# Optimization experiments

Hardware: AMD Instinct MI355X
Metric: run time of the kernel (lower is better)

The kernel has to match this reference:

```python
import jax, jax.numpy as jnp
import numpy as np

HEADS = 5 - 1  # 4 attention heads (GPSConv heads=4)


def _bn(x, g, b, eps=1e-5):
    # BatchNorm1d, training-mode math (biased variance), matches torch normalization
    mu = x.mean(0)
    var = x.var(0)
    return g * (x - mu) * jax.lax.rsqrt(var + eps) + b


def _forward(x, t, freqs, t_fc1_W, t_fc1_b, t_fc2_W, t_fc2_b, node_W, node_b,
             tproj_W, tproj_b, tcat_W, tcat_b, pen_g, pen_b, pel_W, pel_b,
             cat_W, cat_b, conv_Wg, gru_Wih, gru_bih, gru_Whh, gru_bhh,
             attn_Wqkv, attn_bqkv, attn_Wo, attn_bo, bn_g, bn_b,
             mlp_W1, mlp_b1, mlp_W2, mlp_b2, out_W, out_b):
    B, C, Hh, Ww = x.shape
    HD = node_W.shape[1]          # hidden_dim = 64
    DH = HD // HEADS              # per-head dim = 16
    WL = pen_g.shape[0]           # walk_length = 20

    xf = x.reshape(B, -1)                              # [B, D]
    h = xf @ node_W + node_b                           # node_proj

    # TimeEmbedding: t @ freqs -> sin/cos -> MLP, then time_proj
    tp = t.reshape(B, 1) * freqs.reshape(1, -1)        # [B, nf]
    two_pi = jnp.asarray(2.0 * np.pi, x.dtype)
    te = jnp.concatenate([jnp.sin(two_pi * tp), jnp.cos(two_pi * tp)], axis=-1)
    te = jax.nn.silu(te @ t_fc1_W + t_fc1_b) @ t_fc2_W + t_fc2_b
    h_time = te @ tproj_W + tproj_b
    h = jnp.concatenate([h, h_time], axis=-1) @ tcat_W + tcat_b  # time_cat_proj

    # Fully-connected graph incl. self-loops: A = 1 everywhere, deg = B.
    # Random-walk PE: P = A/deg has all entries 1/B; P is idempotent (P@P = P),
    # hence diag(P^k) = diag(P) = 1/B for every k in 1..walk_length.
    A = jnp.ones((B, B), x.dtype)
    P = A / A.sum(1, keepdims=True)
    pe = jnp.broadcast_to(jnp.diagonal(P)[:, None], (B, WL))
    pe = _bn(pe, pen_g, pen_b)                         # pe_norm (batch stats)
    h = jnp.concatenate([h, pe @ pel_W + pel_b], axis=-1) @ cat_W + cat_b

    inv_sqrt = jnp.asarray(1.0 / np.sqrt(DH), x.dtype)
    for l in range(conv_Wg.shape[0]):                  # 5 GPSConv layers
        # --- GatedGraphConv (num_layers=1): message, add-aggregate, GRU ---
        m = A @ (h @ conv_Wg[l])                       # sum of messages from all src nodes
        gi = m @ gru_Wih[l] + gru_bih[l]               # [B, 3H]
        gh = h @ gru_Whh[l] + gru_bhh[l]
        ir, iz, inn = jnp.split(gi, 3, axis=-1)
        hr, hz, hn = jnp.split(gh, 3, axis=-1)
        r = jax.nn.sigmoid(ir + hr)
        z = jax.nn.sigmoid(iz + hz)
        n = jnp.tanh(inn + r * hn)
        hc = (1.0 - z) * n + z * h                     # GRUCell output
        h1 = _bn(hc + h, bn_g[l, 0], bn_b[l, 0])       # residual + norm1

        # --- global multihead self-attention over the single dense batch ---
        qkv = h @ attn_Wqkv[l] + attn_bqkv[l]
        q, k, v = jnp.split(qkv, 3, axis=-1)
        q = q.reshape(B, HEADS, DH).transpose(1, 0, 2)  # [h, B, d]
        k = k.reshape(B, HEADS, DH).transpose(1, 0, 2)
        v = v.reshape(B, HEADS, DH).transpose(1, 0, 2)
        att = jax.nn.softmax(jnp.einsum('hqd,hkd->hqk', q, k) * inv_sqrt, axis=-1)
        o = jnp.einsum('hqk,hkd->hqd', att, v).transpose(1, 0, 2).reshape(B, HD)
        o = o @ attn_Wo[l] + attn_bo[l]
        h2 = _bn(o + h, bn_g[l, 1], bn_b[l, 1])        # residual + norm2

        s = h1 + h2
        s = s + (jax.nn.relu(s @ mlp_W1[l] + mlp_b1[l]) @ mlp_W2[l] + mlp_b2[l])
        h = _bn(s, bn_g[l, 2], bn_b[l, 2])             # norm3

    return (h @ out_W + out_b).reshape(B, C, Hh, Ww)


def setup_inputs() -> dict:
    key = jax.random.key(0)
    B, C, H, W = 2048, 4, 32, 32
    D = C * H * W                 # 4096
    HD, PE, WL, L = 64, 16, 20, 5
    NF, TH, TC = 8, 64, 64
    ks = iter(jax.random.split(key, 40))

    def rn(shape, s=0.05):
        return jax.random.normal(next(ks), shape, jnp.float32) * s

    return {
        'x': jax.random.normal(next(ks), (B, C, H, W), jnp.float32),
        't': jax.random.uniform(next(ks), (B,), jnp.float32),
        'freqs': rn((NF,), 1.0),
        't_fc1_W': rn((2 * NF, TH)), 't_fc1_b': rn((TH,)),
        't_fc2_W': rn((TH, TC)), 't_fc2_b': rn((TC,)),
        'node_W': rn((D, HD), 0.02), 'node_b': rn((HD,)),
        'tproj_W': rn((TC, HD)), 'tproj_b': rn((HD,)),
        'tcat_W': rn((2 * HD, HD)), 'tcat_b': rn((HD,)),
        'pen_g': jnp.ones((WL,), jnp.float32), 'pen_b': jnp.zeros((WL,), jnp.float32),
        'pel_W': rn((WL, PE)), 'pel_b': rn((PE,)),
        'cat_W': rn((HD + PE, HD)), 'cat_b': rn((HD,)),
        'conv_Wg': rn((L, HD, HD)),
        'gru_Wih': rn((L, HD, 3 * HD)), 'gru_bih': rn((L, 3 * HD)),
        'gru_Whh': rn((L, HD, 3 * HD)), 'gru_bhh': rn((L, 3 * HD)),
        'attn_Wqkv': rn((L, HD, 3 * HD)), 'attn_bqkv': rn((L, 3 * HD)),
        'attn_Wo': rn((L, HD, HD)), 'attn_bo': rn((L, HD)),
        'bn_g': jnp.ones((L, 3, HD), jnp.float32), 'bn_b': jnp.zeros((L, 3, HD), jnp.float32),
        'mlp_W1': rn((L, HD, 2 * HD)), 'mlp_b1': rn((L, 2 * HD)),
        'mlp_W2': rn((L, 2 * HD, HD)), 'mlp_b2': rn((L, HD)),
        'out_W': rn((HD, D)), 'out_b': rn((D,)),
    }


def reference(x, t, freqs, t_fc1_W, t_fc1_b, t_fc2_W, t_fc2_b, node_W, node_b,
              tproj_W, tproj_b, tcat_W, tcat_b, pen_g, pen_b, pel_W, pel_b,
              cat_W, cat_b, conv_Wg, gru_Wih, gru_bih, gru_Whh, gru_bhh,
              attn_Wqkv, attn_bqkv, attn_Wo, attn_bo, bn_g, bn_b,
              mlp_W1, mlp_b1, mlp_W2, mlp_b2, out_W, out_b):
    return _forward(x, t, freqs, t_fc1_W, t_fc1_b, t_fc2_W, t_fc2_b, node_W, node_b,
                    tproj_W, tproj_b, tcat_W, tcat_b, pen_g, pen_b, pel_W, pel_b,
                    cat_W, cat_b, conv_Wg, gru_Wih, gru_bih, gru_Whh, gru_bhh,
                    attn_Wqkv, attn_bqkv, attn_Wo, attn_bo, bn_g, bn_b,
                    mlp_W1, mlp_b1, mlp_W2, mlp_b2, out_W, out_b)
```

## Files before the change

### kernel.cpp

```cpp
#include <hip/hip_runtime.h>

#define NB 2048
#define HDM 64
#define NLAY 5

typedef __bf16 bf16x8 __attribute__((ext_vector_type(8)));
typedef float v4f __attribute__((ext_vector_type(4)));

__device__ __forceinline__ float sigmoidf_(float x){ return 1.f/(1.f+__expf(-x)); }
__device__ __forceinline__ float tanhfast_(float x){
  x = fminf(fmaxf(x, -15.f), 15.f);
  float e = __expf(2.f*x);
  return (e-1.f)/(e+1.f);
}
__device__ __forceinline__ unsigned short f2b_rne(float f){
  unsigned u = __float_as_uint(f);
  unsigned r = u + 0x7FFFu + ((u>>16)&1u);
  return (unsigned short)(r>>16);
}
__device__ __forceinline__ unsigned pk2(float a, float b){
  unsigned ua = (__float_as_uint(a) + 0x8000u) >> 16;
  unsigned ub = (__float_as_uint(b) + 0x8000u) & 0xFFFF0000u;
  return ua | ub;
}

__global__ __launch_bounds__(256) void k_pre(
    const float* __restrict__ x, const float* __restrict__ tt,
    const float* __restrict__ freqs,
    const float* __restrict__ fc1W, const float* __restrict__ fc1b,
    const float* __restrict__ fc2W, const float* __restrict__ fc2b,
    const float* __restrict__ tprojW, const float* __restrict__ tprojb,
    const float* __restrict__ nodeW,
    float* __restrict__ h0p, float* __restrict__ htime,
    float* __restrict__ zero_region)
{
  __shared__ float xsT[256*20];
  __shared__ float tb0[128];
  __shared__ float tb1[128];
  const int t = threadIdx.x, blk = blockIdx.x;
  const int r = t>>6, c = t&63;

  if (blk == 0){
    for (int i = t; i < 320 + 1920; i += 256) zero_region[i] = 0.f;
  }

  {
    const int row = blk*2 + (r&1);
    const float tv = tt[row];
    if (r < 2){
      float te[16];
      #pragma unroll
      for (int j=0;j<8;++j){
        float sv, cv;
        __sincosf(6.28318530717958647692f*tv*freqs[j], &sv, &cv);
        te[j]=sv; te[j+8]=cv;
      }
      float a = fc1b[c];
      #pragma unroll
      for (int j=0;j<16;++j) a += te[j]*fc1W[j*64+c];
      tb0[r*64+c] = a*sigmoidf_(a);
    }
    __syncthreads();
    if (r < 2){
      float b2 = fc2b[c];
      #pragma unroll 8
      for (int k=0;k<64;++k) b2 += tb0[r*64+k]*fc2W[k*64+c];
      tb1[r*64+c] = b2;
    }
    __syncthreads();
    if (r < 2){
      float hti = tprojb[c];
      #pragma unroll 8
      for (int k=0;k<64;++k) hti += tb1[r*64+k]*tprojW[k*64+c];
      htime[row*64+c] = hti;
    }
  }

  const int rg = blk>>3, kq = blk&7;
  const int rows0 = rg*16, k0 = kq*512;
  const int col4 = (t&15)*4;
  const int rq4  = ((t>>4)&3)*4;
  const int ksub = (t>>6)*64;

  float4 a0={0,0,0,0}, a1={0,0,0,0}, a2={0,0,0,0}, a3={0,0,0,0};

  for (int ch=0; ch<2; ++ch){
    __syncthreads();
    #pragma unroll
    for (int i=0;i<4;++i){
      int fi = t + 256*i;
      int xr = fi>>6, kk = (fi&63)<<2;
      float4 xv = *(const float4*)&x[(size_t)(rows0+xr)*4096 + k0 + ch*256 + kk];
      xsT[(kk+0)*20+xr]=xv.x; xsT[(kk+1)*20+xr]=xv.y;
      xsT[(kk+2)*20+xr]=xv.z; xsT[(kk+3)*20+xr]=xv.w;
    }
    __syncthreads();
    const float* wp = &nodeW[(size_t)(k0 + ch*256 + ksub)*64 + col4];
    const float* xp = &xsT[ksub*20 + rq4];
    #pragma unroll 8
    for (int kk=0; kk<64; ++kk){
      float4 w  = *(const float4*)&wp[kk*64];
      float4 xr4 = *(const float4*)&xp[kk*20];
      a0.x += xr4.x*w.x; a0.y += xr4.x*w.y; a0.z += xr4.x*w.z; a0.w += xr4.x*w.w;
      a1.x += xr4.y*w.x; a1.y += xr4.y*w.y; a1.z += xr4.y*w.z; a1.w += xr4.y*w.w;
      a2.x += xr4.z*w.x; a2.y += xr4.z*w.y; a2.z += xr4.z*w.z; a2.w += xr4.z*w.w;
      a3.x += xr4.w*w.x; a3.y += xr4.w*w.y; a3.z += xr4.w*w.z; a3.w += xr4.w*w.w;
    }
  }
  __syncthreads();
  {
    const int kqi = t>>6;
    *(float4*)&xsT[(kqi*16 + rq4 + 0)*64 + col4] = a0;
    *(float4*)&xsT[(kqi*16 + rq4 + 1)*64 + col4] = a1;
    *(float4*)&xsT[(kqi*16 + rq4 + 2)*64 + col4] = a2;
    *(float4*)&xsT[(kqi*16 + rq4 + 3)*64 + col4] = a3;
  }
  __syncthreads();
  {
    const int row = t>>4, c4 = (t&15)*4;
    float4 s = {0,0,0,0};
    #pragma unroll
    for (int q=0;q<4;++q){
      float4 v = *(const float4*)&xsT[(q*16+row)*64 + c4];
      s.x+=v.x; s.y+=v.y; s.z+=v.z; s.w+=v.w;
    }
    *(float4*)&h0p[(size_t)kq*(NB*HDM) + (rows0+row)*64 + c4] = s;
  }
}

__global__ __launch_bounds__(256) void k_assemble(
    const float* __restrict__ h0p, const float* __restrict__ htime,
    const float* __restrict__ nodeb,
    const float* __restrict__ tcatW, const float* __restrict__ tcatb,
    const float* __restrict__ penb, const float* __restrict__ pelW,
    const float* __restrict__ pelb,
    const float* __restrict__ catW, const float* __restrict__ catb,
    float* __restrict__ hbuf)
{
  __shared__ float sa[256];
  __shared__ float sb[256];
  __shared__ float cvec[64];
  const int t = threadIdx.x, blk = blockIdx.x;
  const int r = t>>6, c = t&63;
  const int row = blk*4 + r;

  if (r==0){
    float pl[16];
    #pragma unroll
    for (int j=0;j<16;++j){
      float a = pelb[j];
      for (int w=0;w<20;++w) a += penb[w]*pelW[w*16+j];
      pl[j]=a;
    }
    float a = catb[c];
    #pragma unroll
    for (int j=0;j<16;++j) a += pl[j]*catW[(64+j)*64+c];
    cvec[c]=a;
  }
  float h0 = nodeb[c];
  #pragma unroll
  for (int q=0;q<8;++q) h0 += h0p[(size_t)q*(NB*HDM) + row*64 + c];
  sa[t] = h0;
  sb[t] = htime[row*64+c];
  __syncthreads();
  float a = tcatb[c];
  #pragma unroll 4
  for (int k=0;k<64;++k){
    a += sa[r*64+k]*tcatW[k*64+c];
    a += sb[r*64+k]*tcatW[(64+k)*64+c];
  }
  __syncthreads();
  sa[t] = a;
  __syncthreads();
  float hv = cvec[c];
  #pragma unroll 8
  for (int k=0;k<64;++k) hv += sa[r*64+k]*catW[k*64+c];
  hbuf[row*64+c] = hv;
}

__global__ __launch_bounds__(256) void k_A(
    const float* __restrict__ smlp,
    const float* __restrict__ bnaccPrev,
    const float* __restrict__ gPrev, const float* __restrict__ bPrev,
    float* __restrict__ hbuf, float* __restrict__ hsumL,
    const float* __restrict__ Whh, const float* __restrict__ bhh,
    const float* __restrict__ Wq,  const float* __restrict__ bq,
    float* __restrict__ gh,
    unsigned short* __restrict__ Qb, unsigned short* __restrict__ Kb,
    unsigned short* __restrict__ Vt, int first)
{
  __shared__ float sa[256];
  const int t = threadIdx.x, blk = blockIdx.x;
  const int r = t>>6, c = t&63;
  const int row0 = blk*4;
  const int row = row0 + r;

  float hv;
  if (first){
    hv = hbuf[row*64+c];
  } else {
    float mu = bnaccPrev[256+c]*(1.f/NB);
    float va = bnaccPrev[320+c]*(1.f/NB) - mu*mu;
    hv = gPrev[c]*(smlp[row*64+c]-mu)*rsqrtf(va+1e-5f)+bPrev[c];
    hbuf[row*64+c] = hv;
  }
  sa[t] = hv;
  __syncthreads();
  if (t<64){
    atomicAdd(&hsumL[t], sa[t]+sa[64+t]+sa[128+t]+sa[192+t]);
  }
  int rrA[3], ccA[3];
  float ag[3], aq[3];
  #pragma unroll
  for (int i=0;i<3;++i){
    int idx = t + 256*i;
    rrA[i] = idx/192; ccA[i] = idx - rrA[i]*192;
    ag[i] = bhh[ccA[i]]; aq[i] = bq[ccA[i]];
  }
  #pragma unroll 4
  for (int k=0;k<64;++k){
    #pragma unroll
    for (int i=0;i<3;++i){
      float hk = sa[rrA[i]*64+k];
      ag[i] += hk*Whh[k*192+ccA[i]];
      aq[i] += hk*Wq [k*192+ccA[i]];
    }
  }
  #pragma unroll
  for (int i=0;i<3;++i){
    int rw = row0 + rrA[i], cc = ccA[i];
    gh[(size_t)rw*192+cc] = ag[i];
    float aqv = aq[i];
    if (cc < 64){
      int hd = cc>>4, dh = cc&15;
      size_t base = ((size_t)(hd<<11) + rw)*32;
      Qb[base+dh] = f2b_rne(aqv*0.25f);
      Qb[base+16+dh] = 0;
    } else if (cc < 128){
      int c2 = cc-64, hd = c2>>4, dh = c2&15;
      size_t base = ((size_t)(hd<<11) + rw)*32;
      Kb[base+dh] = f2b_rne(aqv);
      Kb[base+16+dh] = 0;
    } else {
      int c2 = cc-128, hd = c2>>4, dh = c2&15;
      Vt[((size_t)(hd*16+dh))*2048 + rw] = f2b_rne(aqv);
    }
  }
}

__global__ __launch_bounds__(64) void k_attn(
    const unsigned short* __restrict__ Qb, const unsigned short* __restrict__ Kb,
    const unsigned short* __restrict__ Vt,
    float* __restrict__ Upart, float* __restrict__ mpart, float* __restrict__ lpart)
{
  __shared__ unsigned short Pl[16*40];
  const int lane = threadIdx.x;
  const int q15 = lane & 15, quad = lane >> 4;
  const int b = blockIdx.x;
  const int qt = b & 127, head = (b>>7)&3, part = b>>9;
  const int qrow = qt*16 + q15;
  const int key00 = part*512;

  const bf16x8 qf = *(const bf16x8*)&Qb[(((size_t)(head<<11))+qrow)*32 + quad*8];
  const unsigned short* Kb_h = Kb + ((size_t)(head<<11))*32;
  const unsigned short* Vrow = Vt + ((size_t)(head*16+q15))*2048;

  v4f O = {0.f,0.f,0.f,0.f};
  float m = -1e30f, lsum = 0.f;

  bf16x8 kf0 = *(const bf16x8*)&Kb_h[(size_t)(key00 + q15)*32 + quad*8];
  bf16x8 kf1 = *(const bf16x8*)&Kb_h[(size_t)(key00 + 16 + q15)*32 + quad*8];
  bf16x8 vf  = *(const bf16x8*)&Vrow[key00 + quad*8];

  for (int c=0; c<16; ++c){
    bf16x8 nk0, nk1, nv;
    if (c < 15){
      int nk = key00 + (c+1)*32;
      nk0 = *(const bf16x8*)&Kb_h[(size_t)(nk + q15)*32 + quad*8];
      nk1 = *(const bf16x8*)&Kb_h[(size_t)(nk + 16 + q15)*32 + quad*8];
      nv  = *(const bf16x8*)&Vrow[nk + quad*8];
    }
    v4f z = {0.f,0.f,0.f,0.f};
    v4f s0 = __builtin_amdgcn_mfma_f32_16x16x32_bf16(kf0, qf, z, 0,0,0);
    v4f s1 = __builtin_amdgcn_mfma_f32_16x16x32_bf16(kf1, qf, z, 0,0,0);
    float cmax = fmaxf(fmaxf(fmaxf(s0[0],s0[1]),fmaxf(s0[2],s0[3])),
                       fmaxf(fmaxf(s1[0],s1[1]),fmaxf(s1[2],s1[3])));
    cmax = fmaxf(cmax, __shfl_xor(cmax,16,64));
    cmax = fmaxf(cmax, __shfl_xor(cmax,32,64));
    float mnew = fmaxf(m, cmax);
    float alpha = __expf(m - mnew);
    float p0=__expf(s0[0]-mnew), p1=__expf(s0[1]-mnew), p2=__expf(s0[2]-mnew), p3=__expf(s0[3]-mnew);
    float p4=__expf(s1[0]-mnew), p5=__expf(s1[1]-mnew), p6=__expf(s1[2]-mnew), p7=__expf(s1[3]-mnew);
    lsum = alpha*lsum + ((p0+p1)+(p2+p3)+((p4+p5)+(p6+p7)));
    m = mnew;
    O[0]*=alpha; O[1]*=alpha; O[2]*=alpha; O[3]*=alpha;
    *(uint2*)&Pl[q15*40 + quad*4]      = make_uint2(pk2(p0,p1), pk2(p2,p3));
    *(uint2*)&Pl[q15*40 + 16 + quad*4] = make_uint2(pk2(p4,p5), pk2(p6,p7));
    __syncthreads();
    bf16x8 pf = *(const bf16x8*)&Pl[q15*40 + quad*8];
    O = __builtin_amdgcn_mfma_f32_16x16x32_bf16(vf, pf, O, 0,0,0);
    kf0 = nk0; kf1 = nk1; vf = nv;
  }
  lsum += __shfl_xor(lsum,16,64);
  lsum += __shfl_xor(lsum,32,64);
  size_t ub = ((size_t)((part*4+head)*2048) + qrow)*16 + quad*4;
  *(float4*)&Upart[ub] = make_float4(O[0],O[1],O[2],O[3]);
  if (quad==0){
    mpart[(size_t)(part*4+head)*2048 + qrow] = m;
    lpart[(size_t)(part*4+head)*2048 + qrow] = lsum;
  }
}

__global__ __launch_bounds__(256) void k_B2(
    const float* __restrict__ hbuf, const float* __restrict__ gh,
    const float* __restrict__ hsumL,
    const float* __restrict__ Upart, const float* __restrict__ mpart,
    const float* __restrict__ lpart,
    const float* __restrict__ Wg,   const float* __restrict__ Wih,
    const float* __restrict__ bih,  const float* __restrict__ Wo,
    const float* __restrict__ bo,
    float* __restrict__ s1, float* __restrict__ s2, float* __restrict__ bnaccL)
{
  __shared__ float sa[256];
  __shared__ float os[256];
  __shared__ float smv_[64];
  __shared__ float sgi[192];
  __shared__ float Sb[512];
  const int t = threadIdx.x, blk = blockIdx.x;
  const int r = t>>6, c = t&63;
  const int row = blk*4 + r;
  const int head = c>>4, dh = c&15;

  if (t<64){
    float a=0.f;
    #pragma unroll 8
    for (int k=0;k<64;++k) a += hsumL[k]*Wg[k*64+t];
    smv_[t]=a;
  }
  sa[t] = hbuf[row*64+c];

  float m0 = mpart[(size_t)(head)*2048+row],    m1 = mpart[(size_t)(4+head)*2048+row];
  float m2 = mpart[(size_t)(8+head)*2048+row],  m3 = mpart[(size_t)(12+head)*2048+row];
  float mm = fmaxf(fmaxf(m0,m1),fmaxf(m2,m3));
  float a0=__expf(m0-mm), a1=__expf(m1-mm), a2=__expf(m2-mm), a3=__expf(m3-mm);
  float ll = a0*lpart[(size_t)(head)*2048+row]   + a1*lpart[(size_t)(4+head)*2048+row]
           + a2*lpart[(size_t)(8+head)*2048+row] + a3*lpart[(size_t)(12+head)*2048+row];
  float uu = a0*Upart[((size_t)(head)*2048+row)*16+dh]    + a1*Upart[((size_t)(4+head)*2048+row)*16+dh]
           + a2*Upart[((size_t)(8+head)*2048+row)*16+dh]  + a3*Upart[((size_t)(12+head)*2048+row)*16+dh];
  os[t] = uu / ll;
  __syncthreads();
  if (t<192){
    float a = bih[t];
    #pragma unroll 8
    for (int k=0;k<64;++k) a += smv_[k]*Wih[k*192+t];
    sgi[t]=a;
  }
  __syncthreads();

  float o2 = bo[c];
  #pragma unroll 8
  for (int k=0;k<64;++k) o2 += os[r*64+k]*Wo[k*64+c];
  float hv = sa[t];
  float s2v = o2 + hv;
  float ir = sgi[c]      + gh[(size_t)row*192+c];
  float iz = sgi[64+c]   + gh[(size_t)row*192+64+c];
  float inn = sgi[128+c];
  float hn  = gh[(size_t)row*192+128+c];
  float rr_ = sigmoidf_(ir);
  float zz  = sigmoidf_(iz);
  float nn  = tanhfast_(inn + rr_*hn);
  float s1v = (1.f-zz)*nn + zz*hv + hv;
  s1[row*64+c] = s1v;
  s2[row*64+c] = s2v;
  Sb[t] = s1v; Sb[256+t] = s2v;
  __syncthreads();
  if (t<64){
    float a=0.f,aq=0.f,b=0.f,bq2=0.f;
    #pragma unroll
    for (int rr=0;rr<4;++rr){
      float v1 = Sb[rr*64+t], v2 = Sb[256+rr*64+t];
      a+=v1; aq+=v1*v1; b+=v2; bq2+=v2*v2;
    }
    atomicAdd(&bnaccL[t],a);     atomicAdd(&bnaccL[64+t],aq);
    atomicAdd(&bnaccL[128+t],b); atomicAdd(&bnaccL[192+t],bq2);
  }
}

__global__ __launch_bounds__(256) void k_C(
    const float* __restrict__ s1, const float* __restrict__ s2,
    const float* __restrict__ bngL, const float* __restrict__ bnbL,
    const float* __restrict__ W1, const float* __restrict__ b1,
    const float* __restrict__ W2, const float* __restrict__ b2,
    float* __restrict__ smlp, float* __restrict__ bnaccL)
{
  __shared__ float sa[256];
  __shared__ float sh[512];
  __shared__ float S2[256];
  const int t = threadIdx.x, blk = blockIdx.x;
  const int r = t>>6, c = t&63;
  const int row = blk*4 + r;

  float mu1 = bnaccL[c]*(1.f/NB);
  float va1 = bnaccL[64+c]*(1.f/NB) - mu1*mu1;
  float mu2 = bnaccL[128+c]*(1.f/NB);
  float va2 = bnaccL[192+c]*(1.f/NB) - mu2*mu2;
  float h1 = bngL[c]*(s1[row*64+c]-mu1)*rsqrtf(va1+1e-5f)+bnbL[c];
  float h2 = bngL[64+c]*(s2[row*64+c]-mu2)*rsqrtf(va2+1e-5f)+bnbL[64+c];
  float sv = h1+h2;
  sa[t]=sv;
  __syncthreads();
  {
    const int rr0 = t>>7, hj0 = t&127;
    const int idx1 = t + 256;
    const int rr1 = idx1>>7, hj1 = idx1&127;
    float a0v = b1[hj0], a1v = b1[hj1];
    #pragma unroll 4
    for (int k=0;k<64;++k){
      a0v += sa[rr0*64+k]*W1[k*128+hj0];
      a1v += sa[rr1*64+k]*W1[k*128+hj1];
    }
    sh[t] = fmaxf(a0v, 0.f);
    sh[t+256] = fmaxf(a1v, 0.f);
  }
  __syncthreads();
  float mo = b2[c];
  #pragma unroll 8
  for (int k=0;k<128;++k) mo += sh[r*128+k]*W2[k*64+c];
  float smv2 = sv + mo;
  smlp[row*64+c]=smv2;
  S2[t]=smv2;
  __syncthreads();
  if (t<64){
    float a=0.f,aq=0.f;
    #pragma unroll
    for (int rr=0;rr<4;++rr){ float v=S2[rr*64+t]; a+=v; aq+=v*v; }
    atomicAdd(&bnaccL[256+t],a); atomicAdd(&bnaccL[320+t],aq);
  }
}

__global__ __launch_bounds__(256) void k_out(
  const float* __restrict__ smlp, const float* __restrict__ bnacc4,
  const float* __restrict__ g4, const float* __restrict__ b4,
  const float* __restrict__ outW, const float* __restrict__ outb,
  float* __restrict__ out)
{
  __shared__ float hsT[64*20];
  const int t = threadIdx.x, blk = blockIdx.x;
  const int rg = blk>>2, cg = blk&3;
  const int rows0 = rg*16;
  #pragma unroll
  for (int i=0;i<4;++i){
    int idx = t + 256*i;
    int k = idx&63, rr = idx>>6;
    float mu = bnacc4[256+k]*(1.f/NB);
    float va = bnacc4[320+k]*(1.f/NB)-mu*mu;
    hsT[k*20+rr] = g4[k]*(smlp[(size_t)(rows0+rr)*64+k]-mu)*rsqrtf(va+1e-5f)+b4[k];
  }
  __syncthreads();
  for (int j=0;j<4;++j){
    int cc = cg*1024 + t + 256*j;
    float acc[16];
    float bv = outb[cc];
    #pragma unroll
    for (int rr=0;rr<16;++rr) acc[rr]=bv;
    #pragma unroll 4
    for (int k=0;k<64;++k){
      float w = outW[(size_t)k*4096+cc];
      const float4* hp = (const float4*)&hsT[k*20];
      float4 h0=hp[0], h1=hp[1], h2=hp[2], h3=hp[3];
      acc[0]+=h0.x*w;  acc[1]+=h0.y*w;  acc[2]+=h0.z*w;  acc[3]+=h0.w*w;
      acc[4]+=h1.x*w;  acc[5]+=h1.y*w;  acc[6]+=h1.z*w;  acc[7]+=h1.w*w;
      acc[8]+=h2.x*w;  acc[9]+=h2.y*w;  acc[10]+=h2.z*w; acc[11]+=h2.w*w;
      acc[12]+=h3.x*w; acc[13]+=h3.y*w; acc[14]+=h3.z*w; acc[15]+=h3.w*w;
    }
    #pragma unroll
    for (int rr=0;rr<16;++rr) out[(size_t)(rows0+rr)*4096+cc]=acc[rr];
  }
}

extern "C" void kernel_launch(void* const* d_in, const int* in_sizes, int n_in,
                              void* d_out, int out_size, void* d_ws, size_t ws_size,
                              hipStream_t stream)
{
  (void)in_sizes; (void)n_in; (void)out_size; (void)ws_size;
  const float* x      = (const float*)d_in[0];
  const float* tt     = (const float*)d_in[1];
  const float* freqs  = (const float*)d_in[2];
  const float* fc1W   = (const float*)d_in[3];
  const float* fc1b   = (const float*)d_in[4];
  const float* fc2W   = (const float*)d_in[5];
  const float* fc2b   = (const float*)d_in[6];
  const float* nodeW  = (const float*)d_in[7];
  const float* nodeb  = (const float*)d_in[8];
  const float* tprojW = (const float*)d_in[9];
  const float* tprojb = (const float*)d_in[10];
  const float* tcatW  = (const float*)d_in[11];
  const float* tcatb  = (const float*)d_in[12];
  const float* penb   = (const float*)d_in[14];
  const float* pelW   = (const float*)d_in[15];
  const float* pelb   = (const float*)d_in[16];
  const float* catW   = (const float*)d_in[17];
  const float* catb   = (const float*)d_in[18];
  const float* convWg = (const float*)d_in[19];
  const float* gruWih = (const float*)d_in[20];
  const float* grubih = (const float*)d_in[21];
  const float* gruWhh = (const float*)d_in[22];
  const float* grubhh = (const float*)d_in[23];
  const float* Wqkv   = (const float*)d_in[24];
  const float* bqkv   = (const float*)d_in[25];
  const float* Wo     = (const float*)d_in[26];
  const float* bo     = (const float*)d_in[27];
  const float* bng    = (const float*)d_in[28];
  const float* bnb    = (const float*)d_in[29];
  const float* W1     = (const float*)d_in[30];
  const float* b1     = (const float*)d_in[31];
  const float* W2     = (const float*)d_in[32];
  const float* b2     = (const float*)d_in[33];
  const float* outW   = (const float*)d_in[34];
  const float* outb   = (const float*)d_in[35];

  float* ws = (float*)d_ws;
  float* htime = ws;
  float* hbuf  = htime + 131072;
  float* gh    = hbuf + 131072;
  float* s1    = gh + 393216;
  float* s2    = s1 + 131072;
  float* smlp  = s2 + 131072;
  float* hsum  = smlp + 131072;
  float* bnacc = hsum + 320;
  float* Upart = bnacc + 1920;
  float* mpart = Upart + 524288;
  float* lpart = mpart + 32768;
  unsigned short* Qb = (unsigned short*)(lpart + 32768);
  unsigned short* Kb = Qb + 262144;
  unsigned short* Vt = Kb + 262144;
  float* h0p = Upart;

  dim3 G(512), Blk(256);

  k_pre<<<dim3(1024), Blk, 0, stream>>>(x, tt, freqs, fc1W, fc1b, fc2W, fc2b,
                                        tprojW, tprojb, nodeW, h0p, htime, hsum);

  k_assemble<<<G, Blk, 0, stream>>>(h0p, htime, nodeb, tcatW, tcatb,
                                    penb, pelW, pelb, catW, catb, hbuf);

  for (int l=0; l<NLAY; ++l){
    const float* bnaccPrev = (l==0) ? bnacc : bnacc + (l-1)*384;
    const float* gPrev = (l==0) ? bng : bng + (l-1)*192 + 128;
    const float* bPrev = (l==0) ? bnb : bnb + (l-1)*192 + 128;
    k_A<<<G, Blk, 0, stream>>>(smlp, bnaccPrev, gPrev, bPrev,
                               hbuf, hsum + l*64,
                               gruWhh + l*12288, grubhh + l*192,
                               Wqkv + l*12288, bqkv + l*192,
                               gh, Qb, Kb, Vt, (l==0) ? 1 : 0);
    k_attn<<<dim3(2048), dim3(64), 0, stream>>>(Qb, Kb, Vt, Upart, mpart, lpart);
    k_B2<<<G, Blk, 0, stream>>>(hbuf, gh, hsum + l*64, Upart, mpart, lpart,
                                convWg + l*4096, gruWih + l*12288, grubih + l*192,
                                Wo + l*4096, bo + l*64,
                                s1, s2, bnacc + l*384);
    k_C<<<G, Blk, 0, stream>>>(s1, s2, bng + l*192, bnb + l*192,
                               W1 + l*8192, b1 + l*128, W2 + l*8192, b2 + l*64,
                               smlp, bnacc + l*384);
  }

  k_out<<<G, Blk, 0, stream>>>(smlp, bnacc + 4*384, bng + 896, bnb + 896,
                               outW, outb, (float*)d_out);
}
```

Baseline: 612.1 us.

## Merge attention split-K in-block, widen row tiles, vectorize node and output GEMMs

Attention now runs the four key partitions as four waves of one 256-thread block and combines the partial softmax results in shared memory, writing normalized outputs directly. This removes the Upart/mpart/lpart round trip through global memory and the combine step in k_B2. k_A, k_B2 and k_C now handle 8 rows per block so each weight load is reused across more rows, at the cost of half as many blocks. k_pre stores x row-major in shared memory instead of transposing it, and k_out uses float4 weight loads and stores. Register pressure rises in the reworked loops, and the lower block counts may leave some compute units idle.

New measurement: 523.5 us. -14.5%, faster.

```diff
diff --git a/kernel.cpp b/kernel.cpp
--- a/kernel.cpp
+++ b/kernel.cpp
@@ -34,7 +34,7 @@
     float* __restrict__ h0p, float* __restrict__ htime,
     float* __restrict__ zero_region)
 {
-  __shared__ float xsT[256*20];
+  __shared__ float xs[16*260];
   __shared__ float tb0[128];
   __shared__ float tb1[128];
   const int t = threadIdx.x, blk = blockIdx.x;
@@ -90,30 +90,31 @@
     for (int i=0;i<4;++i){
       int fi = t + 256*i;
       int xr = fi>>6, kk = (fi&63)<<2;
-      float4 xv = *(const float4*)&x[(size_t)(rows0+xr)*4096 + k0 + ch*256 + kk];
-      xsT[(kk+0)*20+xr]=xv.x; xsT[(kk+1)*20+xr]=xv.y;
-      xsT[(kk+2)*20+xr]=xv.z; xsT[(kk+3)*20+xr]=xv.w;
+      *(float4*)&xs[xr*260+kk] = *(const float4*)&x[(size_t)(rows0+xr)*4096 + k0 + ch*256 + kk];
     }
     __syncthreads();
     const float* wp = &nodeW[(size_t)(k0 + ch*256 + ksub)*64 + col4];
-    const float* xp = &xsT[ksub*20 + rq4];
+    const float* xp = &xs[rq4*260 + ksub];
     #pragma unroll 8
     for (int kk=0; kk<64; ++kk){
       float4 w  = *(const float4*)&wp[kk*64];
-      float4 xr4 = *(const float4*)&xp[kk*20];
-      a0.x += xr4.x*w.x; a0.y += xr4.x*w.y; a0.z += xr4.x*w.z; a0.w += xr4.x*w.w;
-      a1.x += xr4.y*w.x; a1.y += xr4.y*w.y; a1.z += xr4.y*w.z; a1.w += xr4.y*w.w;
-      a2.x += xr4.z*w.x; a2.y += xr4.z*w.y; a2.z += xr4.z*w.z; a2.w += xr4.z*w.w;
-      a3.x += xr4.w*w.x; a3.y += xr4.w*w.y; a3.z += xr4.w*w.z; a3.w += xr4.w*w.w;
+      float x0 = xp[kk];
+      float x1 = xp[260+kk];
+      float x2 = xp[520+kk];
+      float x3 = xp[780+kk];
+      a0.x += x0*w.x; a0.y += x0*w.y; a0.z += x0*w.z; a0.w += x0*w.w;
+      a1.x += x1*w.x; a1.y += x1*w.y; a1.z += x1*w.z; a1.w += x1*w.w;
+      a2.x += x2*w.x; a2.y += x2*w.y; a2.z += x2*w.z; a2.w += x2*w.w;
+      a3.x += x3*w.x; a3.y += x3*w.y; a3.z += x3*w.z; a3.w += x3*w.w;
     }
   }
   __syncthreads();
   {
     const int kqi = t>>6;
-    *(float4*)&xsT[(kqi*16 + rq4 + 0)*64 + col4] = a0;
-    *(float4*)&xsT[(kqi*16 + rq4 + 1)*64 + col4] = a1;
-    *(float4*)&xsT[(kqi*16 + rq4 + 2)*64 + col4] = a2;
-    *(float4*)&xsT[(kqi*16 + rq4 + 3)*64 + col4] = a3;
+    *(float4*)&xs[(kqi*16 + rq4 + 0)*64 + col4] = a0;
+    *(float4*)&xs[(kqi*16 + rq4 + 1)*64 + col4] = a1;
+    *(float4*)&xs[(kqi*16 + rq4 + 2)*64 + col4] = a2;
+    *(float4*)&xs[(kqi*16 + rq4 + 3)*64 + col4] = a3;
   }
   __syncthreads();
   {
@@ -121,7 +122,7 @@
     float4 s = {0,0,0,0};
     #pragma unroll
     for (int q=0;q<4;++q){
-      float4 v = *(const float4*)&xsT[(q*16+row)*64 + c4];
+      float4 v = *(const float4*)&xs[(q*16+row)*64 + c4];
       s.x+=v.x; s.y+=v.y; s.z+=v.z; s.w+=v.w;
     }
     *(float4*)&h0p[(size_t)kq*(NB*HDM) + (rows0+row)*64 + c4] = s;
@@ -189,77 +190,89 @@
     unsigned short* __restrict__ Qb, unsigned short* __restrict__ Kb,
     unsigned short* __restrict__ Vt, int first)
 {
-  __shared__ float sa[256];
+  __shared__ float sa[8*64];
   const int t = threadIdx.x, blk = blockIdx.x;
-  const int r = t>>6, c = t&63;
-  const int row0 = blk*4;
-  const int row = row0 + r;
-
-  float hv;
-  if (first){
-    hv = hbuf[row*64+c];
-  } else {
-    float mu = bnaccPrev[256+c]*(1.f/NB);
-    float va = bnaccPrev[320+c]*(1.f/NB) - mu*mu;
-    hv = gPrev[c]*(smlp[row*64+c]-mu)*rsqrtf(va+1e-5f)+bPrev[c];
-    hbuf[row*64+c] = hv;
-  }
-  sa[t] = hv;
+  const int row0 = blk*8;
+
+  #pragma unroll
+  for (int i=0;i<2;++i){
+    int idx = t + 256*i;
+    int rl = idx>>6, c = idx&63;
+    int row = row0 + rl;
+    float hv;
+    if (first){
+      hv = hbuf[row*64+c];
+    } else {
+      float mu = bnaccPrev[256+c]*(1.f/NB);
+      float va = bnaccPrev[320+c]*(1.f/NB) - mu*mu;
+      hv = gPrev[c]*(smlp[row*64+c]-mu)*rsqrtf(va+1e-5f)+bPrev[c];
+      hbuf[row*64+c] = hv;
+    }
+    sa[idx] = hv;
+  }
   __syncthreads();
   if (t<64){
-    atomicAdd(&hsumL[t], sa[t]+sa[64+t]+sa[128+t]+sa[192+t]);
-  }
-  int rrA[3], ccA[3];
-  float ag[3], aq[3];
-  #pragma unroll
-  for (int i=0;i<3;++i){
-    int idx = t + 256*i;
-    rrA[i] = idx/192; ccA[i] = idx - rrA[i]*192;
-    ag[i] = bhh[ccA[i]]; aq[i] = bq[ccA[i]];
-  }
-  #pragma unroll 4
-  for (int k=0;k<64;++k){
-    #pragma unroll
-    for (int i=0;i<3;++i){
-      float hk = sa[rrA[i]*64+k];
-      ag[i] += hk*Whh[k*192+ccA[i]];
-      aq[i] += hk*Wq [k*192+ccA[i]];
-    }
-  }
-  #pragma unroll
-  for (int i=0;i<3;++i){
-    int rw = row0 + rrA[i], cc = ccA[i];
-    gh[(size_t)rw*192+cc] = ag[i];
-    float aqv = aq[i];
-    if (cc < 64){
-      int hd = cc>>4, dh = cc&15;
-      size_t base = ((size_t)(hd<<11) + rw)*32;
-      Qb[base+dh] = f2b_rne(aqv*0.25f);
-      Qb[base+16+dh] = 0;
-    } else if (cc < 128){
-      int c2 = cc-64, hd = c2>>4, dh = c2&15;
-      size_t base = ((size_t)(hd<<11) + rw)*32;
-      Kb[base+dh] = f2b_rne(aqv);
-      Kb[base+16+dh] = 0;
-    } else {
-      int c2 = cc-128, hd = c2>>4, dh = c2&15;
-      Vt[((size_t)(hd*16+dh))*2048 + rw] = f2b_rne(aqv);
-    }
-  }
-}
-
-__global__ __launch_bounds__(64) void k_attn(
+    float s = 0.f;
+    #pragma unroll
+    for (int rl=0;rl<8;++rl) s += sa[rl*64+t];
+    atomicAdd(&hsumL[t], s);
+  }
+  if (t < 192){
+    const int cc = t;
+    float ag[8], aq[8];
+    float bh = bhh[cc], bq_ = bq[cc];
+    #pragma unroll
+    for (int rl=0;rl<8;++rl){ ag[rl]=bh; aq[rl]=bq_; }
+    #pragma unroll 4
+    for (int k=0;k<64;++k){
+      float wh = Whh[k*192+cc];
+      float wq = Wq [k*192+cc];
+      #pragma unroll
+      for (int rl=0;rl<8;++rl){
+        float hk = sa[rl*64+k];
+        ag[rl] += hk*wh;
+        aq[rl] += hk*wq;
+      }
+    }
+    #pragma unroll
+    for (int rl=0;rl<8;++rl){
+      int rw = row0 + rl;
+      gh[(size_t)rw*192+cc] = ag[rl];
+      float aqv = aq[rl];
+      if (cc < 64){
+        int hd = cc>>4, dh = cc&15;
+        size_t base = ((size_t)(hd<<11) + rw)*32;
+        Qb[base+dh] = f2b_rne(aqv*0.25f);
+        Qb[base+16+dh] = 0;
+      } else if (cc < 128){
+        int c2 = cc-64, hd = c2>>4, dh = c2&15;
+        size_t base = ((size_t)(hd<<11) + rw)*32;
+        Kb[base+dh] = f2b_rne(aqv);
+        Kb[base+16+dh] = 0;
+      } else {
+        int c2 = cc-128, hd = c2>>4, dh = c2&15;
+        Vt[((size_t)(hd*16+dh))*2048 + rw] = f2b_rne(aqv);
+      }
+    }
+  }
+}
+
+__global__ __launch_bounds__(256) void k_attn(
     const unsigned short* __restrict__ Qb, const unsigned short* __restrict__ Kb,
     const unsigned short* __restrict__ Vt,
-    float* __restrict__ Upart, float* __restrict__ mpart, float* __restrict__ lpart)
-{
-  __shared__ unsigned short Pl[16*40];
-  const int lane = threadIdx.x;
+    float* __restrict__ o_out)
+{
+  __shared__ unsigned short Pl[4*640];
+  __shared__ float Os[4*272];
+  __shared__ float ms[64], ls[64];
+  const int t = threadIdx.x;
+  const int w = t>>6, lane = t&63;
   const int q15 = lane & 15, quad = lane >> 4;
   const int b = blockIdx.x;
-  const int qt = b & 127, head = (b>>7)&3, part = b>>9;
+  const int qt = b & 127, head = b>>7;
   const int qrow = qt*16 + q15;
-  const int key00 = part*512;
+  const int key00 = w*512;
+  unsigned short* Plw = &Pl[w*640];
 
   const bf16x8 qf = *(const bf16x8*)&Qb[(((size_t)(head<<11))+qrow)*32 + quad*8];
   const unsigned short* Kb_h = Kb + ((size_t)(head<<11))*32;
@@ -294,42 +307,46 @@
     lsum = alpha*lsum + ((p0+p1)+(p2+p3)+((p4+p5)+(p6+p7)));
     m = mnew;
     O[0]*=alpha; O[1]*=alpha; O[2]*=alpha; O[3]*=alpha;
-    *(uint2*)&Pl[q15*40 + quad*4]      = make_uint2(pk2(p0,p1), pk2(p2,p3));
-    *(uint2*)&Pl[q15*40 + 16 + quad*4] = make_uint2(pk2(p4,p5), pk2(p6,p7));
-    __syncthreads();
-    bf16x8 pf = *(const bf16x8*)&Pl[q15*40 + quad*8];
+    *(uint2*)&Plw[q15*40 + quad*4]      = make_uint2(pk2(p0,p1), pk2(p2,p3));
+    *(uint2*)&Plw[q15*40 + 16 + quad*4] = make_uint2(pk2(p4,p5), pk2(p6,p7));
+    asm volatile("s_waitcnt lgkmcnt(0)" ::: "memory");
+    bf16x8 pf = *(const bf16x8*)&Plw[q15*40 + quad*8];
     O = __builtin_amdgcn_mfma_f32_16x16x32_bf16(vf, pf, O, 0,0,0);
     kf0 = nk0; kf1 = nk1; vf = nv;
   }
   lsum += __shfl_xor(lsum,16,64);
   lsum += __shfl_xor(lsum,32,64);
-  size_t ub = ((size_t)((part*4+head)*2048) + qrow)*16 + quad*4;
-  *(float4*)&Upart[ub] = make_float4(O[0],O[1],O[2],O[3]);
-  if (quad==0){
-    mpart[(size_t)(part*4+head)*2048 + qrow] = m;
-    lpart[(size_t)(part*4+head)*2048 + qrow] = lsum;
+  #pragma unroll
+  for (int j=0;j<4;++j) Os[w*272 + q15*17 + quad*4 + j] = O[j];
+  if (quad==0){ ms[w*16+q15]=m; ls[w*16+q15]=lsum; }
+  __syncthreads();
+  {
+    const int dh = t&15, q = t>>4;
+    float m0=ms[q], m1=ms[16+q], m2=ms[32+q], m3=ms[48+q];
+    float mm = fmaxf(fmaxf(m0,m1),fmaxf(m2,m3));
+    float a0=__expf(m0-mm), a1=__expf(m1-mm), a2=__expf(m2-mm), a3=__expf(m3-mm);
+    float ll = a0*ls[q]+a1*ls[16+q]+a2*ls[32+q]+a3*ls[48+q];
+    float oo = a0*Os[q*17+dh] + a1*Os[272+q*17+dh] + a2*Os[544+q*17+dh] + a3*Os[816+q*17+dh];
+    o_out[(size_t)(qt*16+q)*64 + head*16 + dh] = oo / ll;
   }
 }
 
 __global__ __launch_bounds__(256) void k_B2(
     const float* __restrict__ hbuf, const float* __restrict__ gh,
-    const float* __restrict__ hsumL,
-    const float* __restrict__ Upart, const float* __restrict__ mpart,
-    const float* __restrict__ lpart,
+    const float* __restrict__ hsumL, const float* __restrict__ o_out,
     const float* __restrict__ Wg,   const float* __restrict__ Wih,
     const float* __restrict__ bih,  const float* __restrict__ Wo,
     const float* __restrict__ bo,
     float* __restrict__ s1, float* __restrict__ s2, float* __restrict__ bnaccL)
 {
-  __shared__ float sa[256];
-  __shared__ float os[256];
+  __shared__ float sa[8*64];
+  __shared__ float os[8*64];
   __shared__ float smv_[64];
   __shared__ float sgi[192];
-  __shared__ float Sb[512];
+  __shared__ float Sb1[8*64];
+  __shared__ float Sb2[8*64];
   const int t = threadIdx.x, blk = blockIdx.x;
-  const int r = t>>6, c = t&63;
-  const int row = blk*4 + r;
-  const int head = c>>4, dh = c&15;
+  const int row0 = blk*8;
 
   if (t<64){
     float a=0.f;
@@ -337,17 +354,13 @@
     for (int k=0;k<64;++k) a += hsumL[k]*Wg[k*64+t];
     smv_[t]=a;
   }
-  sa[t] = hbuf[row*64+c];
-
-  float m0 = mpart[(size_t)(head)*2048+row],    m1 = mpart[(size_t)(4+head)*2048+row];
-  float m2 = mpart[(size_t)(8+head)*2048+row],  m3 = mpart[(size_t)(12+head)*2048+row];
-  float mm = fmaxf(fmaxf(m0,m1),fmaxf(m2,m3));
-  float a0=__expf(m0-mm), a1=__expf(m1-mm), a2=__expf(m2-mm), a3=__expf(m3-mm);
-  float ll = a0*lpart[(size_t)(head)*2048+row]   + a1*lpart[(size_t)(4+head)*2048+row]
-           + a2*lpart[(size_t)(8+head)*2048+row] + a3*lpart[(size_t)(12+head)*2048+row];
-  float uu = a0*Upart[((size_t)(head)*2048+row)*16+dh]    + a1*Upart[((size_t)(4+head)*2048+row)*16+dh]
-           + a2*Upart[((size_t)(8+head)*2048+row)*16+dh]  + a3*Upart[((size_t)(12+head)*2048+row)*16+dh];
-  os[t] = uu / ll;
+  #pragma unroll
+  for (int i=0;i<2;++i){
+    int idx = t + 256*i;
+    int rl = idx>>6, c = idx&63;
+    sa[idx] = hbuf[(size_t)(row0+rl)*64+c];
+    os[idx] = o_out[(size_t)(row0+rl)*64+c];
+  }
   __syncthreads();
   if (t<192){
     float a = bih[t];
@@ -357,28 +370,40 @@
   }
   __syncthreads();
 
-  float o2 = bo[c];
-  #pragma unroll 8
-  for (int k=0;k<64;++k) o2 += os[r*64+k]*Wo[k*64+c];
-  float hv = sa[t];
-  float s2v = o2 + hv;
-  float ir = sgi[c]      + gh[(size_t)row*192+c];
-  float iz = sgi[64+c]   + gh[(size_t)row*192+64+c];
-  float inn = sgi[128+c];
-  float hn  = gh[(size_t)row*192+128+c];
-  float rr_ = sigmoidf_(ir);
-  float zz  = sigmoidf_(iz);
-  float nn  = tanhfast_(inn + rr_*hn);
-  float s1v = (1.f-zz)*nn + zz*hv + hv;
-  s1[row*64+c] = s1v;
-  s2[row*64+c] = s2v;
-  Sb[t] = s1v; Sb[256+t] = s2v;
+  const int c = t&63, rg = t>>6;
+  float o2a = bo[c], o2b = bo[c];
+  #pragma unroll 4
+  for (int k=0;k<64;++k){
+    float w = Wo[k*64+c];
+    o2a += os[(rg*2  )*64+k]*w;
+    o2b += os[(rg*2+1)*64+k]*w;
+  }
+  #pragma unroll
+  for (int i=0;i<2;++i){
+    int rl = rg*2 + i;
+    int row = row0 + rl;
+    float o2 = i ? o2b : o2a;
+    float hv = sa[rl*64+c];
+    float s2v = o2 + hv;
+    float ir = sgi[c]      + gh[(size_t)row*192+c];
+    float iz = sgi[64+c]   + gh[(size_t)row*192+64+c];
+    float inn = sgi[128+c];
+    float hn  = gh[(size_t)row*192+128+c];
+    float rr_ = sigmoidf_(ir);
+    float zz  = sigmoidf_(iz);
+    float nn  = tanhfast_(inn + rr_*hn);
+    float s1v = (1.f-zz)*nn + zz*hv + hv;
+    s1[(size_t)row*64+c] = s1v;
+    s2[(size_t)row*64+c] = s2v;
+    Sb1[rl*64+c] = s1v;
+    Sb2[rl*64+c] = s2v;
+  }
   __syncthreads();
   if (t<64){
     float a=0.f,aq=0.f,b=0.f,bq2=0.f;
     #pragma unroll
-    for (int rr=0;rr<4;++rr){
-      float v1 = Sb[rr*64+t], v2 = Sb[256+rr*64+t];
+    for (int rl=0;rl<8;++rl){
+      float v1 = Sb1[rl*64+t], v2 = Sb2[rl*64+t];
       a+=v1; aq+=v1*v1; b+=v2; bq2+=v2*v2;
     }
     atomicAdd(&bnaccL[t],a);     atomicAdd(&bnaccL[64+t],aq);
@@ -393,47 +418,65 @@
     const float* __restrict__ W2, const float* __restrict__ b2,
     float* __restrict__ smlp, float* __restrict__ bnaccL)
 {
-  __shared__ float sa[256];
-  __shared__ float sh[512];
-  __shared__ float S2[256];
+  __shared__ float sa[8*64];
+  __shared__ float sh[8*128];
+  __shared__ float S2[8*64];
   const int t = threadIdx.x, blk = blockIdx.x;
-  const int r = t>>6, c = t&63;
-  const int row = blk*4 + r;
-
-  float mu1 = bnaccL[c]*(1.f/NB);
-  float va1 = bnaccL[64+c]*(1.f/NB) - mu1*mu1;
-  float mu2 = bnaccL[128+c]*(1.f/NB);
-  float va2 = bnaccL[192+c]*(1.f/NB) - mu2*mu2;
-  float h1 = bngL[c]*(s1[row*64+c]-mu1)*rsqrtf(va1+1e-5f)+bnbL[c];
-  float h2 = bngL[64+c]*(s2[row*64+c]-mu2)*rsqrtf(va2+1e-5f)+bnbL[64+c];
-  float sv = h1+h2;
-  sa[t]=sv;
+  const int row0 = blk*8;
+
+  #pragma unroll
+  for (int i=0;i<2;++i){
+    int idx = t + 256*i;
+    int rl = idx>>6, c = idx&63;
+    int row = row0 + rl;
+    float mu1 = bnaccL[c]*(1.f/NB);
+    float va1 = bnaccL[64+c]*(1.f/NB) - mu1*mu1;
+    float mu2 = bnaccL[128+c]*(1.f/NB);
+    float va2 = bnaccL[192+c]*(1.f/NB) - mu2*mu2;
+    float h1 = bngL[c]*(s1[(size_t)row*64+c]-mu1)*rsqrtf(va1+1e-5f)+bnbL[c];
+    float h2 = bngL[64+c]*(s2[(size_t)row*64+c]-mu2)*rsqrtf(va2+1e-5f)+bnbL[64+c];
+    sa[idx] = h1+h2;
+  }
   __syncthreads();
   {
-    const int rr0 = t>>7, hj0 = t&127;
-    const int idx1 = t + 256;
-    const int rr1 = idx1>>7, hj1 = idx1&127;
-    float a0v = b1[hj0], a1v = b1[hj1];
+    const int hj = t&127, rgq = t>>7;
+    float a0v=b1[hj], a1v=b1[hj], a2v=b1[hj], a3v=b1[hj];
     #pragma unroll 4
     for (int k=0;k<64;++k){
-      a0v += sa[rr0*64+k]*W1[k*128+hj0];
-      a1v += sa[rr1*64+k]*W1[k*128+hj1];
-    }
-    sh[t] = fmaxf(a0v, 0.f);
-    sh[t+256] = fmaxf(a1v, 0.f);
-  }
-  __syncthreads();
-  float mo = b2[c];
-  #pragma unroll 8
-  for (int k=0;k<128;++k) mo += sh[r*128+k]*W2[k*64+c];
-  float smv2 = sv + mo;
-  smlp[row*64+c]=smv2;
-  S2[t]=smv2;
+      float w = W1[k*128+hj];
+      a0v += sa[(rgq*4  )*64+k]*w;
+      a1v += sa[(rgq*4+1)*64+k]*w;
+      a2v += sa[(rgq*4+2)*64+k]*w;
+      a3v += sa[(rgq*4+3)*64+k]*w;
+    }
+    sh[(rgq*4  )*128+hj] = fmaxf(a0v,0.f);
+    sh[(rgq*4+1)*128+hj] = fmaxf(a1v,0.f);
+    sh[(rgq*4+2)*128+hj] = fmaxf(a2v,0.f);
+    sh[(rgq*4+3)*128+hj] = fmaxf(a3v,0.f);
+  }
+  __syncthreads();
+  {
+    const int c = t&63, rg = t>>6;
+    float moa = b2[c], mob = b2[c];
+    #pragma unroll 4
+    for (int k=0;k<128;++k){
+      float w = W2[k*64+c];
+      moa += sh[(rg*2  )*128+k]*w;
+      mob += sh[(rg*2+1)*128+k]*w;
+    }
+    #pragma unroll
+    for (int i=0;i<2;++i){
+      int rl = rg*2+i;
+      float smv2 = sa[rl*64+c] + (i ? mob : moa);
+      smlp[(size_t)(row0+rl)*64+c] = smv2;
+      S2[rl*64+c] = smv2;
+    }
+  }
   __syncthreads();
   if (t<64){
     float a=0.f,aq=0.f;
     #pragma unroll
-    for (int rr=0;rr<4;++rr){ float v=S2[rr*64+t]; a+=v; aq+=v*v; }
+    for (int rl=0;rl<8;++rl){ float v=S2[rl*64+t]; a+=v; aq+=v*v; }
     atomicAdd(&bnaccL[256+t],a); atomicAdd(&bnaccL[320+t],aq);
   }
 }
@@ -457,25 +500,38 @@
     hsT[k*20+rr] = g4[k]*(smlp[(size_t)(rows0+rr)*64+k]-mu)*rsqrtf(va+1e-5f)+b4[k];
   }
   __syncthreads();
-  for (int j=0;j<4;++j){
-    int cc = cg*1024 + t + 256*j;
-    float acc[16];
-    float bv = outb[cc];
+  const int cc = cg*1024 + t*4;
+  float4 acc[16];
+  {
+    float4 bv = *(const float4*)&outb[cc];
     #pragma unroll
     for (int rr=0;rr<16;++rr) acc[rr]=bv;
-    #pragma unroll 4
-    for (int k=0;k<64;++k){
-      float w = outW[(size_t)k*4096+cc];
-      const float4* hp = (const float4*)&hsT[k*20];
-      float4 h0=hp[0], h1=hp[1], h2=hp[2], h3=hp[3];
-      acc[0]+=h0.x*w;  acc[1]+=h0.y*w;  acc[2]+=h0.z*w;  acc[3]+=h0.w*w;
-      acc[4]+=h1.x*w;  acc[5]+=h1.y*w;  acc[6]+=h1.z*w;  acc[7]+=h1.w*w;
-      acc[8]+=h2.x*w;  acc[9]+=h2.y*w;  acc[10]+=h2.z*w; acc[11]+=h2.w*w;
-      acc[12]+=h3.x*w; acc[13]+=h3.y*w; acc[14]+=h3.z*w; acc[15]+=h3.w*w;
-    }
-    #pragma unroll
-    for (int rr=0;rr<16;++rr) out[(size_t)(rows0+rr)*4096+cc]=acc[rr];
-  }
+  }
+  #pragma unroll 4
+  for (int k=0;k<64;++k){
+    float4 w = *(const float4*)&outW[(size_t)k*4096+cc];
+    const float4* hp = (const float4*)&hsT[k*20];
+    float4 h0=hp[0], h1=hp[1], h2=hp[2], h3=hp[3];
+    acc[0].x+=h0.x*w.x;  acc[0].y+=h0.x*w.y;  acc[0].z+=h0.x*w.z;  acc[0].w+=h0.x*w.w;
+    acc[1].x+=h0.y*w.x;  acc[1].y+=h0.y*w.y;  acc[1].z+=h0.y*w.z;  acc[1].w+=h0.y*w.w;
+    acc[2].x+=h0.z*w.x;  acc[2].y+=h0.z*w.y;  acc[2].z+=h0.z*w.z;  acc[2].w+=h0.z*w.w;
+    acc[3].x+=h0.w*w.x;  acc[3].y+=h0.w*w.y;  acc[3].z+=h0.w*w.z;  acc[3].w+=h0.w*w.w;
+    acc[4].x+=h1.x*w.x;  acc[4].y+=h1.x*w.y;  acc[4].z+=h1.x*w.z;  acc[4].w+=h1.x*w.w;
+    acc[5].x+=h1.y*w.x;  acc[5].y+=h1.y*w.y;  acc[5].z+=h1.y*w.z;  acc[5].w+=h1.y*w.w;
+    acc[6].x+=h1.z*w.x;  acc[6].y+=h1.z*w.y;  acc[6].z+=h1.z*w.z;  acc[6].w+=h1.z*w.w;
+    acc[7].x+=h1.w*w.x;  acc[7].y+=h1.w*w.y;  acc[7].z+=h1.w*w.z;  acc[7].w+=h1.w*w.w;
+    acc[8].x+=h2.x*w.x;  acc[8].y+=h2.x*w.y;  acc[8].z+=h2.x*w.z;  acc[8].w+=h2.x*w.w;
+    acc[9].x+=h2.y*w.x;  acc[9].y+=h2.y*w.y;  acc[9].z+=h2.y*w.z;  acc[9].w+=h2.y*w.w;
+    acc[10].x+=h2.z*w.x; acc[10].y+=h2.z*w.y; acc[10].z+=h2.z*w.z; acc[10].w+=h2.z*w.w;
+    acc[11].x+=h2.w*w.x; acc[11].y+=h2.w*w.y; acc[11].z+=h2.w*w.z; acc[11].w+=h2.w*w.w;
+    acc[12].x+=h3.x*w.x; acc[12].y+=h3.x*w.y; acc[12].z+=h3.x*w.z; acc[12].w+=h3.x*w.w;
+    acc[13].x+=h3.y*w.x; acc[13].y+=h3.y*w.y; acc[13].z+=h3.y*w.z; acc[13].w+=h3.y*w.w;
+    acc[14].x+=h3.z*w.x; acc[14].y+=h3.z*w.y; acc[14].z+=h3.z*w.z; acc[14].w+=h3.z*w.w;
+    acc[15].x+=h3.w*w.x; acc[15].y+=h3.w*w.y; acc[15].z+=h3.w*w.z; acc[15].w+=h3.w*w.w;
+  }
+  #pragma unroll
+  for (int rr=0;rr<16;++rr)
+    *(float4*)&out[(size_t)(rows0+rr)*4096+cc] = acc[rr];
 }
 
 extern "C" void kernel_launch(void* const* d_in, const int* in_sizes, int n_in,
@@ -526,43 +582,41 @@
   float* s1    = gh + 393216;
   float* s2    = s1 + 131072;
   float* smlp  = s2 + 131072;
-  float* hsum  = smlp + 131072;
+  float* o_out = smlp + 131072;
+  float* hsum  = o_out + 131072;
   float* bnacc = hsum + 320;
-  float* Upart = bnacc + 1920;
-  float* mpart = Upart + 524288;
-  float* lpart = mpart + 32768;
-  unsigned short* Qb = (unsigned short*)(lpart + 32768);
+  unsigned short* Qb = (unsigned short*)(bnacc + 1920);
   unsigned short* Kb = Qb + 262144;
   unsigned short* Vt = Kb + 262144;
-  float* h0p = Upart;
-
-  dim3 G(512), Blk(256);
+  float* h0p  = (float*)(Vt + 65536);
+
+  dim3 Blk(256);
 
   k_pre<<<dim3(1024), Blk, 0, stream>>>(x, tt, freqs, fc1W, fc1b, fc2W, fc2b,
                                         tprojW, tprojb, nodeW, h0p, htime, hsum);
 
-  k_assemble<<<G, Blk, 0, stream>>>(h0p, htime, nodeb, tcatW, tcatb,
-                                    penb, pelW, pelb, catW, catb, hbuf);
+  k_assemble<<<dim3(512), Blk, 0, stream>>>(h0p, htime, nodeb, tcatW, tcatb,
+                                            penb, pelW, pelb, catW, catb, hbuf);
 
   for (int l=0; l<NLAY; ++l){
     const float* bnaccPrev = (l==0) ? bnacc : bnacc + (l-1)*384;
     const float* gPrev = (l==0) ? bng : bng + (l-1)*192 + 128;
     const float* bPrev = (l==0) ? bnb : bnb + (l-1)*192 + 128;
-    k_A<<<G, Blk, 0, stream>>>(smlp, bnaccPrev, gPrev, bPrev,
-                               hbuf, hsum + l*64,
-                               gruWhh + l*12288, grubhh + l*192,
-                               Wqkv + l*12288, bqkv + l*192,
-                               gh, Qb, Kb, Vt, (l==0) ? 1 : 0);
-    k_attn<<<dim3(2048), dim3(64), 0, stream>>>(Qb, Kb, Vt, Upart, mpart, lpart);
-    k_B2<<<G, Blk, 0, stream>>>(hbuf, gh, hsum + l*64, Upart, mpart, lpart,
-                                convWg + l*4096, gruWih + l*12288, grubih + l*192,
-                                Wo + l*4096, bo + l*64,
-                                s1, s2, bnacc + l*384);
-    k_C<<<G, Blk, 0, stream>>>(s1, s2, bng + l*192, bnb + l*192,
-                               W1 + l*8192, b1 + l*128, W2 + l*8192, b2 + l*64,
-                               smlp, bnacc + l*384);
-  }
-
-  k_out<<<G, Blk, 0, stream>>>(smlp, bnacc + 4*384, bng + 896, bnb + 896,
-                               outW, outb, (float*)d_out);
-}
+    k_A<<<dim3(256), Blk, 0, stream>>>(smlp, bnaccPrev, gPrev, bPrev,
+                                       hbuf, hsum + l*64,
+                                       gruWhh + l*12288, grubhh + l*192,
+                                       Wqkv + l*12288, bqkv + l*192,
+                                       gh, Qb, Kb, Vt, (l==0) ? 1 : 0);
+    k_attn<<<dim3(512), Blk, 0, stream>>>(Qb, Kb, Vt, o_out);
+    k_B2<<<dim3(256), Blk, 0, stream>>>(hbuf, gh, hsum + l*64, o_out,
+                                        convWg + l*4096, gruWih + l*12288, grubih + l*192,
+                                        Wo + l*4096, bo + l*64,
+                                        s1, s2, bnacc + l*384);
+    k_C<<<dim3(256), Blk, 0, stream>>>(s1, s2, bng + l*192, bnb + l*192,
+                                       W1 + l*8192, b1 + l*128, W2 + l*8192, b2 + l*64,
+                                       smlp, bnacc + l*384);
+  }
+
+  k_out<<<dim3(512), Blk, 0, stream>>>(smlp, bnacc + 4*384, bng + 896, bnb + 896,
+                                       outW, outb, (float*)d_out);
+}
```
